# Kernel tuning notes

Measured on AMD Instinct MI355X. Metric: run time of the kernel, lower is better.

## Reference

```python
import jax, jax.numpy as jnp
import numpy as np

B = 100_000   # graph nodes in batch
C = 1_000     # virtual-node clusters
D = 512       # in_dim (attention hidden dim)
OUT = 512     # out_dim


def setup_inputs() -> dict:
    key = jax.random.key(0)
    ks = jax.random.split(key, 9)
    h = jax.random.normal(ks[0], (B, D), dtype=jnp.float32)
    g = jax.random.normal(ks[1], (C, D), dtype=jnp.float32)
    # vn_index[:,1] is the cluster id of node i; arange%C guarantees every
    # cluster is present, so the per-cluster concat has exactly C rows in
    # sorted-cluster-id order (matching torch .unique() iteration order).
    vn_index = jnp.stack([jnp.arange(B, dtype=jnp.int32),
                          jnp.arange(B, dtype=jnp.int32) % C], axis=1)
    n_id = jnp.arange(B, dtype=jnp.int32)
    s = 1.0 / np.sqrt(D)
    Wq = jax.random.uniform(ks[2], (D, D), jnp.float32, -s, s)   # query_proj (no bias)
    Wk = jax.random.uniform(ks[3], (D, D), jnp.float32, -s, s)   # key_proj (no bias)
    attn_bias = jax.random.uniform(ks[4], (D,), jnp.float32, -0.1, 0.1)
    Ws = jax.random.uniform(ks[5], (1, D), jnp.float32, -s, s)   # score_proj weight
    bs = jax.random.uniform(ks[6], (1,), jnp.float32, -s, s)     # score_proj bias
    so = 1.0 / np.sqrt(D)
    W = jax.random.uniform(ks[7], (OUT, D), jnp.float32, -so, so)  # final Linear
    b = jax.random.uniform(ks[8], (OUT,), jnp.float32, -so, so)
    return {"h": h, "g": g, "vn_index": vn_index, "n_id": n_id,
            "Wq": Wq, "Wk": Wk, "attn_bias": attn_bias, "Ws": Ws, "bs": bs,
            "W": W, "b": b}


def reference(h, g, vn_index, n_id, Wq, Wk, attn_bias, Ws, bs, W, b):
    # cluster id for each batch node (B,)
    cluster = vn_index[n_id, 1]
    # additive attention, vectorized over all nodes (replaces per-cluster loop)
    qp = g @ Wq.T                                   # (C, D) query proj per cluster
    kp = h @ Wk.T                                   # (B, D) key proj per node
    score = jnp.tanh(kp + qp[cluster] + attn_bias) @ Ws[0] + bs[0]  # (B,)
    # segment softmax over each cluster
    smax = jax.ops.segment_max(score, cluster, num_segments=C)      # (C,)
    e = jnp.exp(score - smax[cluster])                              # (B,)
    denom = jax.ops.segment_sum(e, cluster, num_segments=C)         # (C,)
    attn = e / denom[cluster]                                       # (B,)
    # attention-weighted sum of node features per cluster -> (C, D)
    ctx = jax.ops.segment_sum(attn[:, None] * h, cluster, num_segments=C)
    # final projection + tanh activation -> (C, OUT)
    return jnp.tanh(ctx @ W.T + b)
```

## Files before the change

kernel.cpp:

```cpp
#include <hip/hip_runtime.h>
#include <stdint.h>

#define D_DIM 512

typedef __attribute__((ext_vector_type(8))) short bf16x8;
typedef __attribute__((ext_vector_type(4))) float f32x4;
typedef __attribute__((ext_vector_type(4))) short short4_t;
typedef __attribute__((ext_vector_type(4))) float float4_t;

__device__ __forceinline__ unsigned short f2bf(float f) {
  unsigned u = __float_as_uint(f);
  u += 0x7FFFu + ((u >> 16) & 1u);
  return (unsigned short)(u >> 16);
}

__device__ __forceinline__ float bf2f(unsigned short s) {
  return __uint_as_float(((unsigned)s) << 16);
}

__device__ __forceinline__ float tanh_fast(float x) {
  float e = __expf(2.0f * x);
  return 1.0f - 2.0f / (e + 1.0f);
}

#define GLOAD_LDS16(gsrc, ldst) \
  __builtin_amdgcn_global_load_lds((const __attribute__((address_space(1))) void*)(gsrc), \
                                   (__attribute__((address_space(3))) void*)(ldst), 16, 0, 0)


__global__ void cvt_f32_bf16_k(const float* __restrict__ in, unsigned short* __restrict__ out, int n4) {
  int i = blockIdx.x * blockDim.x + threadIdx.x;
  if (i < n4) {
    float4_t v = ((const float4_t*)in)[i];
    short4_t s;
    s.x = (short)f2bf(v.x); s.y = (short)f2bf(v.y);
    s.z = (short)f2bf(v.z); s.w = (short)f2bf(v.w);
    ((short4_t*)out)[i] = s;
  }
}

__global__ void cvt3_f32_bf16_k(const float* __restrict__ a, const float* __restrict__ b,
                                const float* __restrict__ c, unsigned short* __restrict__ out,
                                int n4each) {
  int i = blockIdx.x * blockDim.x + threadIdx.x;
  if (i >= 3 * n4each) return;
  int sel = i / n4each, j = i - sel * n4each;
  const float* src = (sel == 0) ? a : (sel == 1) ? b : c;
  float4_t v = ((const float4_t*)src)[j];
  short4_t s;
  s.x = (short)f2bf(v.x); s.y = (short)f2bf(v.y);
  s.z = (short)f2bf(v.z); s.w = (short)f2bf(v.w);
  ((short4_t*)out)[i] = s;
}

__global__ void prep_cluster_k(const int* __restrict__ vn, const int* __restrict__ nid,
                               int* __restrict__ cl, int* __restrict__ counts, int B) {
  int i = blockIdx.x * blockDim.x + threadIdx.x;
  if (i < B) {
    int c = vn[2 * nid[i] + 1];
    cl[i] = c;
    atomicAdd(&counts[c], 1);
  }
}

__global__ void prefix_k(const int* __restrict__ counts, int* __restrict__ starts,
                         int* __restrict__ cursor, int C) {
  __shared__ int sh[1024];
  int t = threadIdx.x;
  int v = (t < C) ? counts[t] : 0;
  sh[t] = v;
  __syncthreads();
  for (int off = 1; off < 1024; off <<= 1) {
    int x = (t >= off) ? sh[t - off] : 0;
    __syncthreads();
    sh[t] += x;
    __syncthreads();
  }
  if (t < C) { int st = sh[t] - v; starts[t] = st; cursor[t] = st; }
  if (t == 1023) starts[C] = sh[1023];
}

__global__ void scatter_k(const int* __restrict__ cl, int* __restrict__ cursor,
                          int* __restrict__ order, int B) {
  int i = blockIdx.x * blockDim.x + threadIdx.x;
  if (i < B) {
    int pos = atomicAdd(&cursor[cl[i]], 1);
    order[pos] = i;
  }
}

__device__ __forceinline__ unsigned enc_f(float f) {
  unsigned u = __float_as_uint(f);
  return (u & 0x80000000u) ? ~u : (u | 0x80000000u);
}
__device__ __forceinline__ float dec_f(unsigned u) {
  return __uint_as_float((u & 0x80000000u) ? (u & 0x7FFFFFFFu) : ~u);
}

__global__ void seg_max_k(const float* __restrict__ score, const int* __restrict__ cl,
                          unsigned* __restrict__ smax, int B) {
  int i = blockIdx.x * blockDim.x + threadIdx.x;
  if (i < B) atomicMax(&smax[cl[i]], enc_f(score[i]));
}

__global__ void seg_expsum_k(const float* __restrict__ score, const int* __restrict__ cl,
                             const unsigned* __restrict__ smax, float* __restrict__ ev,
                             float* __restrict__ denom, int B) {
  int i = blockIdx.x * blockDim.x + threadIdx.x;
  if (i < B) {
    int c = cl[i];
    float x = __expf(score[i] - dec_f(smax[c]));
    ev[i] = x;
    atomicAdd(&denom[c], x);
  }
}

__global__ __launch_bounds__(256)
void ctx_k(const unsigned short* __restrict__ hbf, const float* __restrict__ ev,
           const int* __restrict__ order, const int* __restrict__ starts,
           const float* __restrict__ denom, float* __restrict__ ctx) {
  int c = blockIdx.x;
  int t = threadIdx.x;
  int s0 = starts[c], s1 = starts[c + 1];
  float a0 = 0.f, a1 = 0.f;
  int j = s0;
  for (; j + 3 < s1; j += 4) {
    int i0 = order[j], i1 = order[j + 1], i2 = order[j + 2], i3 = order[j + 3];
    float e0 = ev[i0], e1 = ev[i1], e2 = ev[i2], e3 = ev[i3];
    unsigned u0 = *(const unsigned*)(hbf + (size_t)i0 * D_DIM + t * 2);
    unsigned u1 = *(const unsigned*)(hbf + (size_t)i1 * D_DIM + t * 2);
    unsigned u2 = *(const unsigned*)(hbf + (size_t)i2 * D_DIM + t * 2);
    unsigned u3 = *(const unsigned*)(hbf + (size_t)i3 * D_DIM + t * 2);
    a0 += e0 * bf2f((unsigned short)u0) + e1 * bf2f((unsigned short)u1)
        + e2 * bf2f((unsigned short)u2) + e3 * bf2f((unsigned short)u3);
    a1 += e0 * bf2f((unsigned short)(u0 >> 16)) + e1 * bf2f((unsigned short)(u1 >> 16))
        + e2 * bf2f((unsigned short)(u2 >> 16)) + e3 * bf2f((unsigned short)(u3 >> 16));
  }
  for (; j < s1; ++j) {
    int i0 = order[j];
    float e0 = ev[i0];
    unsigned u0 = *(const unsigned*)(hbf + (size_t)i0 * D_DIM + t * 2);
    a0 += e0 * bf2f((unsigned short)u0);
    a1 += e0 * bf2f((unsigned short)(u0 >> 16));
  }
  float inv = 1.0f / denom[c];
  float2 r = make_float2(a0 * inv, a1 * inv);
  *(float2*)(&ctx[(size_t)c * D_DIM + t * 2]) = r;
}

template<int EPI>
__global__ __launch_bounds__(256)
void gemm128_k(const unsigned short* __restrict__ Abf,
               const unsigned short* __restrict__ Bw, int M,
               const float* __restrict__ qb, const int* __restrict__ cl,
               const float* __restrict__ Ws, const float* __restrict__ bias,
               float* __restrict__ out)
{
  __shared__ unsigned short As[2][128 * 32];
  __shared__ unsigned short Bs[2][128 * 32];
  __shared__ float red[128][2];
  __shared__ int clds[128];

  const int t = threadIdx.x;
  const int lane = t & 63;
  const int w = t >> 6;
  const int wr = w >> 1, wc = w & 1;
  const int l15 = lane & 15, l4 = lane >> 4;

  const int nwg = gridDim.x;
  int id = blockIdx.x;
  if ((nwg & 7) == 0) id = (id & 7) * (nwg >> 3) + (id >> 3);
  const int n0 = (id & 3) * 128;
  const int m0 = (id >> 2) * 128;

  if (EPI == 1 && t < 128) {
    int gm = m0 + t;
    clds[t] = (gm < M) ? cl[gm] : 0;
  }
  __builtin_amdgcn_sched_barrier(0);

  const int rin = lane >> 2;
  const int sl = lane & 3;

  const unsigned short* srcA[2];
  const unsigned short* srcB[2];
  int dstOff[2];
  #pragma unroll
  for (int c = 0; c < 2; ++c) {
    int chunk = w * 2 + c;
    int row = chunk * 16 + rin;
    int slot = sl ^ ((row ^ (row >> 2)) & 3);
    int ga = m0 + row; if (ga > M - 1) ga = M - 1;
    srcA[c] = Abf + (size_t)ga * 512 + slot * 8;
    srcB[c] = Bw + (size_t)(n0 + row) * 512 + slot * 8;
    dstOff[c] = chunk * 1024;
  }

  int offA[4], offB[4];
  #pragma unroll
  for (int mi = 0; mi < 4; ++mi) {
    int row = wr * 64 + mi * 16 + l15;
    offA[mi] = row * 64 + ((l4 ^ ((row ^ (row >> 2)) & 3)) * 16);
  }
  #pragma unroll
  for (int ni = 0; ni < 4; ++ni) {
    int row = wc * 64 + ni * 16 + l15;
    offB[ni] = row * 64 + ((l4 ^ ((row ^ (row >> 2)) & 3)) * 16);
  }

  f32x4 acc[4][4];
  #pragma unroll
  for (int mi = 0; mi < 4; ++mi)
    #pragma unroll
    for (int ni = 0; ni < 4; ++ni)
      acc[mi][ni] = (f32x4){0.f, 0.f, 0.f, 0.f};

  #pragma unroll
  for (int c = 0; c < 2; ++c) {
    GLOAD_LDS16(srcA[c], ((char*)As[0]) + dstOff[c]);
    GLOAD_LDS16(srcB[c], ((char*)Bs[0]) + dstOff[c]);
  }
  __builtin_amdgcn_sched_barrier(0);

  #pragma unroll
  for (int it = 0; it < 16; ++it) {
    const int cur = it & 1;
    if (it < 15) {
      const int k1 = (it + 1) * 32;
      #pragma unroll
      for (int c = 0; c < 2; ++c) {
        GLOAD_LDS16(srcA[c] + k1, ((char*)As[cur ^ 1]) + dstOff[c]);
        GLOAD_LDS16(srcB[c] + k1, ((char*)Bs[cur ^ 1]) + dstOff[c]);
      }
      __builtin_amdgcn_sched_barrier(0);
      asm volatile("s_waitcnt vmcnt(4)" ::: "memory");
    } else {
      asm volatile("s_waitcnt vmcnt(0)" ::: "memory");
    }
    __builtin_amdgcn_sched_barrier(0);
    __builtin_amdgcn_s_barrier();
    __builtin_amdgcn_sched_barrier(0);

    {
      bf16x8 af[4], bfv[4];
      #pragma unroll
      for (int mi = 0; mi < 4; ++mi)
        af[mi] = *(const bf16x8*)(((const char*)As[cur]) + offA[mi]);
      #pragma unroll
      for (int ni = 0; ni < 4; ++ni)
        bfv[ni] = *(const bf16x8*)(((const char*)Bs[cur]) + offB[ni]);
      #pragma unroll
      for (int mi = 0; mi < 4; ++mi)
        #pragma unroll
        for (int ni = 0; ni < 4; ++ni)
          acc[mi][ni] = __builtin_amdgcn_mfma_f32_16x16x32_bf16(af[mi], bfv[ni], acc[mi][ni], 0, 0, 0);
    }
    __builtin_amdgcn_sched_barrier(0);
    __builtin_amdgcn_s_barrier();
    __builtin_amdgcn_sched_barrier(0);
  }

  if (EPI == 0 || EPI == 2) {
    #pragma unroll
    for (int mi = 0; mi < 4; ++mi) {
      #pragma unroll
      for (int r = 0; r < 4; ++r) {
        int gm = m0 + wr * 64 + mi * 16 + l4 * 4 + r;
        if (gm < M) {
          #pragma unroll
          for (int ni = 0; ni < 4; ++ni) {
            int gcol = n0 + wc * 64 + ni * 16 + l15;
            float v = acc[mi][ni][r] + bias[gcol];
            if (EPI == 2) v = tanh_fast(v);
            out[(size_t)gm * 512 + gcol] = v;
          }
        }
      }
    }
  } else {
    #pragma unroll
    for (int mi = 0; mi < 4; ++mi) {
      #pragma unroll
      for (int r = 0; r < 4; ++r) {
        int rowt = wr * 64 + mi * 16 + l4 * 4 + r;
        int c = clds[rowt];
        const float* qrow = &qb[(size_t)c * 512 + n0 + wc * 64];
        float s = 0.f;
        #pragma unroll
        for (int ni = 0; ni < 4; ++ni) {
          int colw = ni * 16 + l15;
          float x = acc[mi][ni][r] + qrow[colw];
          s += tanh_fast(x) * Ws[n0 + wc * 64 + colw];
        }
        s += __shfl_xor(s, 1);
        s += __shfl_xor(s, 2);
        s += __shfl_xor(s, 4);
        s += __shfl_xor(s, 8);
        if (l15 == 0) red[rowt][wc] = s;
      }
    }
    __syncthreads();
    if (t < 128) {
      int gm = m0 + t;
      if (gm < M) atomicAdd(&out[gm], red[t][0] + red[t][1]);
    }
  }
}


extern "C" void kernel_launch(void* const* d_in, const int* in_sizes, int n_in,
                              void* d_out, int out_size, void* d_ws, size_t ws_size,
                              hipStream_t stream) {
  const float* h  = (const float*)d_in[0];
  const float* g  = (const float*)d_in[1];
  const int*   vn = (const int*)d_in[2];
  const int*   nid= (const int*)d_in[3];
  const float* Wq = (const float*)d_in[4];
  const float* Wk = (const float*)d_in[5];
  const float* ab = (const float*)d_in[6];
  const float* Ws = (const float*)d_in[7];
  const float* W  = (const float*)d_in[9];
  const float* b  = (const float*)d_in[10];

  const int B = in_sizes[3];
  const int C = in_sizes[1] / D_DIM;

  char* wsb = (char*)d_ws;
  size_t off = 0;
  auto alloc = [&](size_t bytes) -> void* {
    void* p = wsb + off;
    off += (bytes + 255) & ~(size_t)255;
    return p;
  };

  unsigned short* hbf   = (unsigned short*)alloc((size_t)B * 512 * 2);
  unsigned short* gbf   = (unsigned short*)alloc((size_t)C * 512 * 2);
  unsigned short* ctxbf = (unsigned short*)alloc((size_t)C * 512 * 2);
  unsigned short* Wk_bf = (unsigned short*)alloc((size_t)512 * 512 * 2);
  unsigned short* Wq_bf = (unsigned short*)alloc((size_t)512 * 512 * 2);
  unsigned short* W_bf  = (unsigned short*)alloc((size_t)512 * 512 * 2);
  float* qb    = (float*)alloc((size_t)C * 512 * 4);
  float* ctx   = (float*)alloc((size_t)C * 512 * 4);
  float* score = (float*)alloc((size_t)B * 4);
  float* ev    = (float*)alloc((size_t)B * 4);
  int*   cl    = (int*)alloc((size_t)B * 4);
  int*   order = (int*)alloc((size_t)B * 4);
  int*      counts = (int*)alloc((size_t)C * 4);
  unsigned* smax   = (unsigned*)alloc((size_t)C * 4);
  float*    denom  = (float*)alloc((size_t)C * 4);
  int* starts = (int*)alloc((size_t)(C + 1) * 4);
  int* cursor = (int*)alloc((size_t)C * 4);
  (void)ws_size; (void)n_in; (void)out_size;

  size_t zlen = (size_t)((char*)denom - (char*)counts) + (size_t)C * 4;
  hipMemsetAsync(counts, 0, zlen, stream);
  hipMemsetAsync(score, 0, (size_t)B * 4, stream);

  cvt_f32_bf16_k<<<(B * 512 / 4 + 255) / 256, 256, 0, stream>>>(h, hbf, B * 512 / 4);
  cvt_f32_bf16_k<<<(C * 512 / 4 + 255) / 256, 256, 0, stream>>>(g, gbf, C * 512 / 4);
  const int n4w = 512 * 512 / 4;
  cvt3_f32_bf16_k<<<(3 * n4w + 255) / 256, 256, 0, stream>>>(Wk, Wq, W, Wk_bf, n4w);

  prep_cluster_k<<<(B + 255) / 256, 256, 0, stream>>>(vn, nid, cl, counts, B);
  prefix_k<<<1, 1024, 0, stream>>>(counts, starts, cursor, C);
  scatter_k<<<(B + 255) / 256, 256, 0, stream>>>(cl, cursor, order, B);

  gemm128_k<0><<<4 * ((C + 127) / 128), 256, 0, stream>>>(
      gbf, Wq_bf, C, nullptr, nullptr, nullptr, ab, qb);

  gemm128_k<1><<<4 * ((B + 127) / 128), 256, 0, stream>>>(
      hbf, Wk_bf, B, qb, cl, Ws, nullptr, score);

  seg_max_k<<<(B + 255) / 256, 256, 0, stream>>>(score, cl, smax, B);
  seg_expsum_k<<<(B + 255) / 256, 256, 0, stream>>>(score, cl, smax, ev, denom, B);
  ctx_k<<<C, 256, 0, stream>>>(hbf, ev, order, starts, denom, ctx);

  cvt_f32_bf16_k<<<(C * 512 / 4 + 255) / 256, 256, 0, stream>>>(ctx, ctxbf, C * 512 / 4);

  gemm128_k<2><<<4 * ((C + 127) / 128), 256, 0, stream>>>(
      ctxbf, W_bf, C, nullptr, nullptr, nullptr, b, (float*)d_out);
}
```

Before: 242.6 us.

## Replace score GEMM with 256x256-tile 512-thread kernel using BK=64 pipelining

The large h@Wk^T GEMM with fused tanh-score epilogue moves to a new kernel using 256x256 output tiles, 8 waves, K-step 64 with double-buffered direct-to-LDS loads, XOR swizzle, setprio around MFMA, and a non-power-of-two XCD remap. Larger tiles raise arithmetic intensity, halving redundant A reloads (2 column tiles instead of 4) and cutting the atomic adds per row. It uses 128KB of LDS, which limits occupancy to one block per CU, and puts 128 accumulator registers in each thread. The old templated kernel loses its score epilogue path.

```diff
diff --git a/kernel.cpp b/kernel.cpp
--- a/kernel.cpp
+++ b/kernel.cpp
@@ -148,18 +148,171 @@
   *(float2*)(&ctx[(size_t)c * D_DIM + t * 2]) = r;
 }
 
+__global__ __launch_bounds__(512, 2)
+void gemm256_score_k(const unsigned short* __restrict__ Abf,
+                     const unsigned short* __restrict__ Bw, int M,
+                     const float* __restrict__ qb, const int* __restrict__ cl,
+                     const float* __restrict__ Ws, float* __restrict__ out)
+{
+  __shared__ unsigned short AB[65536];
+  __shared__ float red[256][4];
+  __shared__ int clds[256];
+
+  const int t = threadIdx.x;
+  const int lane = t & 63;
+  const int w = t >> 6;
+  const int wr = w >> 2, wc = w & 3;
+  const int l15 = lane & 15, l4 = lane >> 4;
+
+  const int nwg = gridDim.x;
+  {
+  }
+  int id;
+  {
+    int q = nwg >> 3, r = nwg & 7;
+    int xcd = blockIdx.x & 7, pos = blockIdx.x >> 3;
+    id = (xcd < r ? xcd * (q + 1) : r * (q + 1) + (xcd - r) * q) + pos;
+  }
+  const int n0 = (id & 1) * 256;
+  const int m0 = (id >> 1) * 256;
+
+  if (t < 256) {
+    int gm = m0 + t;
+    clds[t] = (gm < M) ? cl[gm < M ? gm : M - 1] : cl[M - 1];
+  }
+  __builtin_amdgcn_sched_barrier(0);
+
+  const int rin = lane >> 3;
+  const int sl = lane & 7;
+  const int sslot = sl ^ rin;
+
+  const unsigned short* srcA[4];
+  const unsigned short* srcB[4];
+  int chunkOff[4];
+  #pragma unroll
+  for (int c = 0; c < 4; ++c) {
+    int chunk = w * 4 + c;
+    int rowA = m0 + chunk * 8 + rin; if (rowA > M - 1) rowA = M - 1;
+    int colB = n0 + chunk * 8 + rin;
+    srcA[c] = Abf + (size_t)rowA * 512 + sslot * 8;
+    srcB[c] = Bw + (size_t)colB * 512 + sslot * 8;
+    chunkOff[c] = chunk * 1024;
+  }
+
+  int rowA_off[8], rowB_off[4];
+  #pragma unroll
+  for (int mi = 0; mi < 8; ++mi) rowA_off[mi] = (wr * 128 + mi * 16 + l15) * 128;
+  #pragma unroll
+  for (int ni = 0; ni < 4; ++ni) rowB_off[ni] = (wc * 64 + ni * 16 + l15) * 128;
+  int psk[2];
+  psk[0] = ((l4) ^ (l15 & 7)) * 16;
+  psk[1] = ((4 + l4) ^ (l15 & 7)) * 16;
+
+  f32x4 acc[8][4];
+  #pragma unroll
+  for (int mi = 0; mi < 8; ++mi)
+    #pragma unroll
+    for (int ni = 0; ni < 4; ++ni)
+      acc[mi][ni] = (f32x4){0.f, 0.f, 0.f, 0.f};
+
+  #pragma unroll
+  for (int c = 0; c < 4; ++c)
+    GLOAD_LDS16(srcA[c], ((char*)AB) + chunkOff[c]);
+  #pragma unroll
+  for (int c = 0; c < 4; ++c)
+    GLOAD_LDS16(srcB[c], ((char*)AB) + 65536 + chunkOff[c]);
+  __builtin_amdgcn_sched_barrier(0);
+
+  #pragma unroll
+  for (int kt = 0; kt < 8; ++kt) {
+    const int buf = kt & 1;
+    const char* Au = ((const char*)AB) + buf * 32768;
+    const char* Bu = ((const char*)AB) + 65536 + buf * 32768;
+    char* AuN = ((char*)AB) + (buf ^ 1) * 32768;
+    char* BuN = ((char*)AB) + 65536 + (buf ^ 1) * 32768;
+
+    asm volatile("s_waitcnt vmcnt(0)" ::: "memory");
+    __builtin_amdgcn_sched_barrier(0);
+    __builtin_amdgcn_s_barrier();
+    __builtin_amdgcn_sched_barrier(0);
+
+    #pragma unroll
+    for (int ks = 0; ks < 2; ++ks) {
+      bf16x8 a[8], b[4];
+      #pragma unroll
+      for (int mi = 0; mi < 8; ++mi)
+        a[mi] = *(const bf16x8*)(Au + rowA_off[mi] + psk[ks]);
+      #pragma unroll
+      for (int ni = 0; ni < 4; ++ni)
+        b[ni] = *(const bf16x8*)(Bu + rowB_off[ni] + psk[ks]);
+
+      if (kt < 7) {
+        const int k1 = (kt + 1) * 64;
+        if (ks == 0) {
+          #pragma unroll
+          for (int c = 0; c < 4; ++c)
+            GLOAD_LDS16(srcA[c] + k1, AuN + chunkOff[c]);
+        } else {
+          #pragma unroll
+          for (int c = 0; c < 4; ++c)
+            GLOAD_LDS16(srcB[c] + k1, BuN + chunkOff[c]);
+        }
+      }
+      __builtin_amdgcn_sched_barrier(0);
+
+      __builtin_amdgcn_s_setprio(1);
+      #pragma unroll
+      for (int mi = 0; mi < 8; ++mi)
+        #pragma unroll
+        for (int ni = 0; ni < 4; ++ni)
+          acc[mi][ni] = __builtin_amdgcn_mfma_f32_16x16x32_bf16(a[mi], b[ni], acc[mi][ni], 0, 0, 0);
+      __builtin_amdgcn_s_setprio(0);
+      __builtin_amdgcn_sched_barrier(0);
+
+      if (ks == 0) {
+        __builtin_amdgcn_s_barrier();
+        __builtin_amdgcn_sched_barrier(0);
+      }
+    }
+  }
+
+  __syncthreads();
+  #pragma unroll
+  for (int mi = 0; mi < 8; ++mi) {
+    #pragma unroll
+    for (int r = 0; r < 4; ++r) {
+      int rowt = wr * 128 + mi * 16 + l4 * 4 + r;
+      int c = clds[rowt];
+      const float* qrow = &qb[(size_t)c * 512];
+      float s = 0.f;
+      #pragma unroll
+      for (int ni = 0; ni < 4; ++ni) {
+        int gcol = n0 + wc * 64 + ni * 16 + l15;
+        float x = acc[mi][ni][r] + qrow[gcol];
+        s += tanh_fast(x) * Ws[gcol];
+      }
+      s += __shfl_xor(s, 1);
+      s += __shfl_xor(s, 2);
+      s += __shfl_xor(s, 4);
+      s += __shfl_xor(s, 8);
+      if (l15 == 0) red[rowt][wc] = s;
+    }
+  }
+  __syncthreads();
+  if (t < 256) {
+    int gm = m0 + t;
+    if (gm < M) atomicAdd(&out[gm], red[t][0] + red[t][1] + red[t][2] + red[t][3]);
+  }
+}
+
 template<int EPI>
 __global__ __launch_bounds__(256)
 void gemm128_k(const unsigned short* __restrict__ Abf,
                const unsigned short* __restrict__ Bw, int M,
-               const float* __restrict__ qb, const int* __restrict__ cl,
-               const float* __restrict__ Ws, const float* __restrict__ bias,
-               float* __restrict__ out)
+               const float* __restrict__ bias, float* __restrict__ out)
 {
   __shared__ unsigned short As[2][128 * 32];
   __shared__ unsigned short Bs[2][128 * 32];
-  __shared__ float red[128][2];
-  __shared__ int clds[128];
 
   const int t = threadIdx.x;
   const int lane = t & 63;
@@ -172,12 +325,6 @@
   if ((nwg & 7) == 0) id = (id & 7) * (nwg >> 3) + (id >> 3);
   const int n0 = (id & 3) * 128;
   const int m0 = (id >> 2) * 128;
-
-  if (EPI == 1 && t < 128) {
-    int gm = m0 + t;
-    clds[t] = (gm < M) ? cl[gm] : 0;
-  }
-  __builtin_amdgcn_sched_barrier(0);
 
   const int rin = lane >> 2;
   const int sl = lane & 3;
@@ -260,49 +407,20 @@
     __builtin_amdgcn_sched_barrier(0);
   }
 
-  if (EPI == 0 || EPI == 2) {
+  #pragma unroll
+  for (int mi = 0; mi < 4; ++mi) {
     #pragma unroll
-    for (int mi = 0; mi < 4; ++mi) {
-      #pragma unroll
-      for (int r = 0; r < 4; ++r) {
-        int gm = m0 + wr * 64 + mi * 16 + l4 * 4 + r;
-        if (gm < M) {
-          #pragma unroll
-          for (int ni = 0; ni < 4; ++ni) {
-            int gcol = n0 + wc * 64 + ni * 16 + l15;
-            float v = acc[mi][ni][r] + bias[gcol];
-            if (EPI == 2) v = tanh_fast(v);
-            out[(size_t)gm * 512 + gcol] = v;
-          }
+    for (int r = 0; r < 4; ++r) {
+      int gm = m0 + wr * 64 + mi * 16 + l4 * 4 + r;
+      if (gm < M) {
+        #pragma unroll
+        for (int ni = 0; ni < 4; ++ni) {
+          int gcol = n0 + wc * 64 + ni * 16 + l15;
+          float v = acc[mi][ni][r] + bias[gcol];
+          if (EPI == 2) v = tanh_fast(v);
+          out[(size_t)gm * 512 + gcol] = v;
         }
       }
-    }
-  } else {
-    #pragma unroll
-    for (int mi = 0; mi < 4; ++mi) {
-      #pragma unroll
-      for (int r = 0; r < 4; ++r) {
-        int rowt = wr * 64 + mi * 16 + l4 * 4 + r;
-        int c = clds[rowt];
-        const float* qrow = &qb[(size_t)c * 512 + n0 + wc * 64];
-        float s = 0.f;
-        #pragma unroll
-        for (int ni = 0; ni < 4; ++ni) {
-          int colw = ni * 16 + l15;
-          float x = acc[mi][ni][r] + qrow[colw];
-          s += tanh_fast(x) * Ws[n0 + wc * 64 + colw];
-        }
-        s += __shfl_xor(s, 1);
-        s += __shfl_xor(s, 2);
-        s += __shfl_xor(s, 4);
-        s += __shfl_xor(s, 8);
-        if (l15 == 0) red[rowt][wc] = s;
-      }
-    }
-    __syncthreads();
-    if (t < 128) {
-      int gm = m0 + t;
-      if (gm < M) atomicAdd(&out[gm], red[t][0] + red[t][1]);
     }
   }
 }
@@ -365,11 +483,10 @@
   prefix_k<<<1, 1024, 0, stream>>>(counts, starts, cursor, C);
   scatter_k<<<(B + 255) / 256, 256, 0, stream>>>(cl, cursor, order, B);
 
-  gemm128_k<0><<<4 * ((C + 127) / 128), 256, 0, stream>>>(
-      gbf, Wq_bf, C, nullptr, nullptr, nullptr, ab, qb);
-
-  gemm128_k<1><<<4 * ((B + 127) / 128), 256, 0, stream>>>(
-      hbf, Wk_bf, B, qb, cl, Ws, nullptr, score);
+  gemm128_k<0><<<4 * ((C + 127) / 128), 256, 0, stream>>>(gbf, Wq_bf, C, ab, qb);
+
+  gemm256_score_k<<<2 * ((B + 255) / 256), 512, 0, stream>>>(
+      hbf, Wk_bf, B, qb, cl, Ws, score);
 
   seg_max_k<<<(B + 255) / 256, 256, 0, stream>>>(score, cl, smax, B);
   seg_expsum_k<<<(B + 255) / 256, 256, 0, stream>>>(score, cl, smax, ev, denom, B);
@@ -377,6 +494,5 @@
 
   cvt_f32_bf16_k<<<(C * 512 / 4 + 255) / 256, 256, 0, stream>>>(ctx, ctxbf, C * 512 / 4);
 
-  gemm128_k<2><<<4 * ((C + 127) / 128), 256, 0, stream>>>(
-      ctxbf, W_bf, C, nullptr, nullptr, nullptr, b, (float*)d_out);
-}
+  gemm128_k<2><<<4 * ((C + 127) / 128), 256, 0, stream>>>(ctxbf, W_bf, C, b, (float*)d_out);
+}
```

Result: slower. 248.8 us (+2.6%).
